# Kernel tuning notes

Hardware: AMD Instinct MI355X
Metric: run time of the kernel (lower is better)

## Reference

```python
import jax, jax.numpy as jnp
import numpy as np
import math

B, S, I, H = 64, 512, 512, 1024


def setup_inputs() -> dict:
    key = jax.random.key(0)
    kx, k1, k2, k3, k4 = jax.random.split(key, 5)
    stdv = 1.0 / math.sqrt(H)
    x = jax.random.normal(kx, (B, S, I), dtype=jnp.float32)
    w_ih = jax.random.uniform(k1, (4 * H, I), jnp.float32, -stdv, stdv)
    w_hh = jax.random.uniform(k2, (4 * H, H), jnp.float32, -stdv, stdv)
    b_ih = jax.random.uniform(k3, (4 * H,), jnp.float32, -stdv, stdv)
    b_hh = jax.random.uniform(k4, (4 * H,), jnp.float32, -stdv, stdv)
    return {"x": x, "w_ih": w_ih, "w_hh": w_hh, "b_ih": b_ih, "b_hh": b_hh}


def reference(x, w_ih, w_hh, b_ih, b_hh):
    # x: [B,S,I]; w_ih: [4H,I]; w_hh: [4H,H]; biases: [4H]
    Bsz, Ssz, _ = x.shape
    Hsz = w_hh.shape[1]
    # Precompute input contribution for all timesteps in one big GEMM.
    gx = jnp.einsum('bsi,gi->sbg', x, w_ih) + b_ih + b_hh  # [S,B,4H]

    def step(carry, gx_t):
        h, c = carry  # [B,H] each
        gates = gx_t + h @ w_hh.T  # [B,4H]
        i_t, f_t, g_t, o_t = jnp.split(gates, 4, axis=-1)
        i_t = jax.nn.sigmoid(i_t)
        f_t = jax.nn.sigmoid(f_t)
        g_t = jnp.tanh(g_t)
        o_t = jax.nn.sigmoid(o_t)
        c_new = f_t * c + i_t * g_t
        h_new = o_t * jnp.tanh(c_new)
        return (h_new, c_new), h_new

    h0 = jnp.zeros((Bsz, Hsz), dtype=x.dtype)
    c0 = jnp.zeros((Bsz, Hsz), dtype=x.dtype)
    (h_f, c_f), hidden_seq = jax.lax.scan(step, (h0, c0), gx)
    # hidden_seq: [S,B,H] (torch code cats along dim 0 of [1,B,H] slices)
    return hidden_seq, (h_f[None], c_f[None])
```

## Files before the change

### kernel.cpp

```cpp
#include <hip/hip_runtime.h>

typedef _Float16 f16;
typedef _Float16 f16x4 __attribute__((ext_vector_type(4)));
typedef _Float16 f16x8 __attribute__((ext_vector_type(8)));
typedef float f32x4 __attribute__((ext_vector_type(4)));

#define S_LEN 512
#define BSZ 64
#define ISZ 512
#define HSZ 1024

__device__ __forceinline__ float fast_sigmoid(float x) {
  return 1.f / (1.f + __expf(-x));
}
__device__ __forceinline__ float fast_tanh(float x) {
  float t = __expf(-2.f * fabsf(x));
  float r = (1.f - t) / (1.f + t);
  return copysignf(r, x);
}

template<int OFF>
__device__ __forceinline__ void ldg16_sc1(f16x8& d, const f16* p) {
  asm volatile("global_load_dwordx4 %0, %1, off offset:%2 sc1"
               : "=v"(d) : "v"(p), "i"(OFF));
}
__device__ __forceinline__ void st16_sc1(f16* p, f16x8 v) {
  asm volatile("global_store_dwordx4 %0, %1, off sc1" :: "v"(p), "v"(v) : "memory");
}
__device__ __forceinline__ int ld_flag_sc1(const int* p) {
  int v;
  asm volatile("global_load_dword %0, %1, off sc1\n\ts_waitcnt vmcnt(0)"
               : "=v"(v) : "v"(p) : "memory");
  return v;
}
__device__ __forceinline__ void st_flag_sc1(int* p, int v) {
  asm volatile("global_store_dword %0, %1, off sc1" :: "v"(p), "v"(v) : "memory");
}

__global__ void k_cvt(const float* __restrict__ src, f16* __restrict__ dst, int n4) {
  int i = blockIdx.x * blockDim.x + threadIdx.x;
  if (i < n4) {
    float4 v = ((const float4*)src)[i];
    f16x4 h = { (f16)v.x, (f16)v.y, (f16)v.z, (f16)v.w };
    ((f16x4*)dst)[i] = h;
  }
}

__global__ void k_pack_whh(const float* __restrict__ whh, f16* __restrict__ wp) {
  int i = blockIdx.x * blockDim.x + threadIdx.x;
  int idx4 = i * 4;
  int k = idx4 & (HSZ - 1);
  int P = idx4 >> 10;
  int cls = P & 3, u = (P >> 2) & 3, v = (P >> 4) & 7, w = P >> 7;
  int srow = cls * HSZ + w * 32 + v * 4 + u;
  float4 val = *(const float4*)&whh[(size_t)srow * HSZ + k];
  f16x4 h = { (f16)val.x, (f16)val.y, (f16)val.z, (f16)val.w };
  *(f16x4*)&wp[(size_t)P * HSZ + k] = h;
}

__global__ void k_misc(const float* __restrict__ bih, const float* __restrict__ bhh,
                       float* __restrict__ bsum, f16* __restrict__ hbuf,
                       int* __restrict__ bar) {
  int i = blockIdx.x * blockDim.x + threadIdx.x;
  if (i < 4096) bsum[i] = bih[i] + bhh[i];
  if (i < BSZ * HSZ) hbuf[i] = (f16)0.f;
  if (i < 1024) bar[i] = 0;
}

__global__ __launch_bounds__(256) void k_gemm_gx(
    const f16* __restrict__ xh, const f16* __restrict__ wh,
    const float* __restrict__ bsum, f16* __restrict__ gxp)
{
  __shared__ f16 As[128][40];
  __shared__ f16 Bs[128][40];
  const int bn = blockIdx.x, bm = blockIdx.y;
  const int tid = threadIdx.x;
  const int wid = tid >> 6, lane = tid & 63;
  const int wy = wid >> 1, wx = wid & 1;
  const int l15 = lane & 15, lq = lane >> 4;
  const int sr = tid >> 2, sc = (tid & 3) * 8;
  f32x4 acc[4][4] = {};
  const size_t arow = (size_t)bm * 128;
  const size_t brow = (size_t)bn * 128;
  for (int k0 = 0; k0 < ISZ; k0 += 32) {
    __syncthreads();
    *(f16x8*)&As[sr][sc]      = *(const f16x8*)&xh[(arow + sr) * ISZ + k0 + sc];
    *(f16x8*)&As[sr + 64][sc] = *(const f16x8*)&xh[(arow + sr + 64) * ISZ + k0 + sc];
    *(f16x8*)&Bs[sr][sc]      = *(const f16x8*)&wh[(brow + sr) * ISZ + k0 + sc];
    *(f16x8*)&Bs[sr + 64][sc] = *(const f16x8*)&wh[(brow + sr + 64) * ISZ + k0 + sc];
    __syncthreads();
    f16x8 af[4], bf[4];
    #pragma unroll
    for (int t = 0; t < 4; t++) af[t] = *(const f16x8*)&As[wy * 64 + t * 16 + l15][lq * 8];
    #pragma unroll
    for (int t = 0; t < 4; t++) bf[t] = *(const f16x8*)&Bs[wx * 64 + t * 16 + l15][lq * 8];
    #pragma unroll
    for (int mt = 0; mt < 4; mt++)
      #pragma unroll
      for (int nt = 0; nt < 4; nt++)
        acc[mt][nt] = __builtin_amdgcn_mfma_f32_16x16x32_f16(af[mt], bf[nt], acc[mt][nt], 0, 0, 0);
  }
  #pragma unroll
  for (int nt = 0; nt < 4; nt++) {
    const int n = bn * 128 + wx * 64 + nt * 16 + l15;
    const float bs = bsum[n];
    const int cls = n >> 10, j = n & 1023;
    const int w = j >> 5, v = (j >> 2) & 7, u = j & 3;
    #pragma unroll
    for (int mt = 0; mt < 4; mt++) {
      const int m0 = bm * 128 + wy * 64 + mt * 16 + lq * 4;
      #pragma unroll
      for (int r = 0; r < 4; r++) {
        const int m = m0 + r;
        const int b = m >> 9, s = m & 511;
        const int g = b >> 3, bl = b & 7;
        gxp[(((size_t)s * 8 + g) * 32 + w) * 1024 + v * 128 + bl * 16 + u * 4 + cls]
            = (f16)(acc[mt][nt][r] + bs);
      }
    }
  }
}

__global__ __launch_bounds__(512, 2) void k_lstm(
    const f16* __restrict__ wp, const f16* __restrict__ gxp,
    f16* __restrict__ hbuf, int* __restrict__ bar, float* __restrict__ out)
{
  __shared__ __align__(16) f16 hs[8192];
  __shared__ __align__(16) float pre[8][16][12];
  __shared__ __align__(16) f16 hpub[256];
  __shared__ f16 lds_pad[40960];
  const int wg = blockIdx.x;
  const int g  = wg & 7;
  const int w  = wg >> 3;
  const int tid = threadIdx.x;
  const int lane = tid & 63;
  const int wid = tid >> 6;
  const int l15 = lane & 15, lq = lane >> 4;
  const int hr = l15 & 7;
  int* flags = &bar[g * 32];
  lds_pad[tid] = (f16)0.f;

  f16x8 wv[32];
  {
    const f16* wsrc = wp + (size_t)(w * 128 + wid * 16 + l15) * HSZ + lq * 8;
    #pragma unroll
    for (int t = 0; t < 32; t++) wv[t] = *(const f16x8*)(wsrc + t * 32);
  }

  const int fidx = 2 * wid + (lane & 1) + ((lane >> 1) & 1) * 16;
  const int* fp = &flags[fidx];
  int* myflag = &flags[w];

  const int eb = lane >> 2, eu = lane & 3;
  float creg = 0.f;
  float hval = 0.f, cval = 0.f;
  const size_t hseq = (size_t)S_LEN * BSZ * HSZ;
  int p = 0;
  for (int s = 0; s < S_LEN; s++) {
    f16x4 gxv = {};
    if (lane < 32)
      gxv = *(const f16x4*)&gxp[(((size_t)s * 8 + g) * 32 + w) * 1024
                                + wid * 128 + lane * 4];
    for (;;) {
      int v = 0x7fffffff;
      if (lane < 4) v = ld_flag_sc1(fp);
      if (__all(v >= s)) break;
      __builtin_amdgcn_s_sleep(1);
    }
    {
      const f16* hsrc = hbuf + ((size_t)p * 8 + g) * 8192 + (size_t)tid * 8;
      f16x8 s0, s1;
      ldg16_sc1<0>(s0, hsrc);
      ldg16_sc1<0>(s1, hsrc + 4096);
      asm volatile("s_waitcnt vmcnt(0)" : "+v"(s0), "+v"(s1) :: "memory");
      *(f16x8*)&hs[tid * 8] = s0;
      *(f16x8*)&hs[tid * 8 + 4096] = s1;
    }
    asm volatile("s_waitcnt lgkmcnt(0)\n\ts_barrier" ::: "memory");
    f32x4 a0 = {}, a1 = {}, a2 = {}, a3 = {};
    #pragma unroll
    for (int t = 0; t < 32; t += 4) {
      f16x8 h0 = *(const f16x8*)&hs[(t + 0) * 256 + hr * 32 + lq * 8];
      f16x8 h1 = *(const f16x8*)&hs[(t + 1) * 256 + hr * 32 + lq * 8];
      f16x8 h2 = *(const f16x8*)&hs[(t + 2) * 256 + hr * 32 + lq * 8];
      f16x8 h3 = *(const f16x8*)&hs[(t + 3) * 256 + hr * 32 + lq * 8];
      a0 = __builtin_amdgcn_mfma_f32_16x16x32_f16(h0, wv[t + 0], a0, 0, 0, 0);
      a1 = __builtin_amdgcn_mfma_f32_16x16x32_f16(h1, wv[t + 1], a1, 0, 0, 0);
      a2 = __builtin_amdgcn_mfma_f32_16x16x32_f16(h2, wv[t + 2], a2, 0, 0, 0);
      a3 = __builtin_amdgcn_mfma_f32_16x16x32_f16(h3, wv[t + 3], a3, 0, 0, 0);
    }
    f32x4 accs = (a0 + a1) + (a2 + a3);
    if (lq < 2)
      *(f32x4*)&pre[wid][l15][lq * 4] = accs;
    asm volatile("s_waitcnt lgkmcnt(0)" ::: "memory");
    if (lane < 32) {
      const float p0 = pre[wid][eu * 4 + 0][eb] + (float)gxv[0];
      const float p1 = pre[wid][eu * 4 + 1][eb] + (float)gxv[1];
      const float p2 = pre[wid][eu * 4 + 2][eb] + (float)gxv[2];
      const float p3 = pre[wid][eu * 4 + 3][eb] + (float)gxv[3];
      const float ig = fast_sigmoid(p0);
      const float fg = fast_sigmoid(p1);
      const float gg = fast_tanh(p2);
      const float og = fast_sigmoid(p3);
      creg = fg * creg + ig * gg;
      const float h = og * fast_tanh(creg);
      hval = h; cval = creg;
      hpub[eb * 32 + wid * 4 + eu] = (f16)h;
      out[((size_t)s * BSZ + g * 8 + eb) * HSZ + w * 32 + wid * 4 + eu] = h;
      if (s == S_LEN - 1) {
        const int b = g * 8 + eb, J = w * 32 + wid * 4 + eu;
        out[hseq + (size_t)b * HSZ + J] = hval;
        out[hseq + (size_t)BSZ * HSZ + (size_t)b * HSZ + J] = cval;
      }
    }
    asm volatile("s_waitcnt lgkmcnt(0)\n\ts_barrier" ::: "memory");
    if (wid == 0 && s + 1 < S_LEN) {
      if (lane < 32) {
        f16x8 hv = *(const f16x8*)&hpub[lane * 8];
        st16_sc1(&hbuf[((size_t)(p ^ 1) * 8 + g) * 8192 + w * 256 + lane * 8], hv);
      }
      asm volatile("s_waitcnt vmcnt(0)" ::: "memory");
      if (lane == 0) st_flag_sc1(myflag, s + 1);
    }
    p ^= 1;
  }
}

extern "C" void kernel_launch(void* const* d_in, const int* in_sizes, int n_in,
                              void* d_out, int out_size, void* d_ws, size_t ws_size,
                              hipStream_t stream) {
  const float* x   = (const float*)d_in[0];
  const float* wih = (const float*)d_in[1];
  const float* whh = (const float*)d_in[2];
  const float* bih = (const float*)d_in[3];
  const float* bhh = (const float*)d_in[4];
  float* out = (float*)d_out;
  char* ws = (char*)d_ws;
  f16*   xh    = (f16*)(ws + 0);
  f16*   wih_h = (f16*)(ws + 33554432);
  f16*   wp    = (f16*)(ws + 37748736);
  float* bsum  = (float*)(ws + 46137344);
  f16*   hbuf  = (f16*)(ws + 46153728);
  f16*   gxp   = (f16*)(ws + 46415872);
  int*   bar   = (int*)(ws + 314851328);

  k_cvt<<<16384, 256, 0, stream>>>(x, xh, (BSZ * S_LEN * ISZ) / 4);
  k_cvt<<<2048, 256, 0, stream>>>(wih, wih_h, (4 * HSZ * ISZ) / 4);
  k_pack_whh<<<4096, 256, 0, stream>>>(whh, wp);
  k_misc<<<256, 256, 0, stream>>>(bih, bhh, bsum, hbuf, bar);
  dim3 g1(32, 256);
  k_gemm_gx<<<g1, 256, 0, stream>>>(xh, wih_h, bsum, gxp);
  void* args[] = { (void*)&wp, (void*)&gxp, (void*)&hbuf, (void*)&bar, (void*)&out };
  hipLaunchCooperativeKernel((void*)k_lstm, dim3(256), dim3(512), args, 0, stream);
}
```

Baseline: 2.592 ms.

## Split LSTM recurrent GEMM along K across waves, load h fragments directly from global

Each wave now owns a K-slice of the hidden state and computes all 128 gate columns for that slice. It loads its A-fragments directly from the global h buffer into registers instead of staging the whole h vector through LDS, and it issues the gx load alongside them. Partial sums from all 8 waves are reduced through a larger LDS buffer plus a cross-half shuffle. This removes the global-to-LDS copy, one barrier and the LDS padding used to cap occupancy, but adds a cross-wave reduction and reorganises the flag polling.

```diff
diff --git a/kernel.cpp b/kernel.cpp
--- a/kernel.cpp
+++ b/kernel.cpp
@@ -4,6 +4,7 @@
 typedef _Float16 f16x4 __attribute__((ext_vector_type(4)));
 typedef _Float16 f16x8 __attribute__((ext_vector_type(8)));
 typedef float f32x4 __attribute__((ext_vector_type(4)));
+typedef int i32x2 __attribute__((ext_vector_type(2)));
 
 #define S_LEN 512
 #define BSZ 64
@@ -19,11 +20,6 @@
   return copysignf(r, x);
 }
 
-template<int OFF>
-__device__ __forceinline__ void ldg16_sc1(f16x8& d, const f16* p) {
-  asm volatile("global_load_dwordx4 %0, %1, off offset:%2 sc1"
-               : "=v"(d) : "v"(p), "i"(OFF));
-}
 __device__ __forceinline__ void st16_sc1(f16* p, f16x8 v) {
   asm volatile("global_store_dwordx4 %0, %1, off sc1" :: "v"(p), "v"(v) : "memory");
 }
@@ -35,6 +31,18 @@
 }
 __device__ __forceinline__ void st_flag_sc1(int* p, int v) {
   asm volatile("global_store_dword %0, %1, off sc1" :: "v"(p), "v"(v) : "memory");
+}
+__device__ __forceinline__ void ld_afrags(f16x8& a0, f16x8& a1, f16x8& a2, f16x8& a3,
+                                          i32x2& gx, const f16* ap, const f16* gp) {
+  asm volatile(
+    "global_load_dwordx4 %0, %5, off sc1\n\t"
+    "global_load_dwordx4 %1, %5, off offset:512 sc1\n\t"
+    "global_load_dwordx4 %2, %5, off offset:1024 sc1\n\t"
+    "global_load_dwordx4 %3, %5, off offset:1536 sc1\n\t"
+    "global_load_dwordx2 %4, %6, off\n\t"
+    "s_waitcnt vmcnt(1)"
+    : "=&v"(a0), "=&v"(a1), "=&v"(a2), "=&v"(a3), "=&v"(gx)
+    : "v"(ap), "v"(gp) : "memory");
 }
 
 __global__ void k_cvt(const float* __restrict__ src, f16* __restrict__ dst, int n4) {
@@ -125,10 +133,8 @@
     const f16* __restrict__ wp, const f16* __restrict__ gxp,
     f16* __restrict__ hbuf, int* __restrict__ bar, float* __restrict__ out)
 {
-  __shared__ __align__(16) f16 hs[8192];
-  __shared__ __align__(16) float pre[8][16][12];
+  __shared__ __align__(16) float pre[8][128][12];
   __shared__ __align__(16) f16 hpub[256];
-  __shared__ f16 lds_pad[40960];
   const int wg = blockIdx.x;
   const int g  = wg & 7;
   const int w  = wg >> 3;
@@ -136,81 +142,87 @@
   const int lane = tid & 63;
   const int wid = tid >> 6;
   const int l15 = lane & 15, lq = lane >> 4;
-  const int hr = l15 & 7;
+  const int hr8 = l15 & 7;
   int* flags = &bar[g * 32];
-  lds_pad[tid] = (f16)0.f;
 
   f16x8 wv[32];
   {
-    const f16* wsrc = wp + (size_t)(w * 128 + wid * 16 + l15) * HSZ + lq * 8;
-    #pragma unroll
-    for (int t = 0; t < 32; t++) wv[t] = *(const f16x8*)(wsrc + t * 32);
-  }
-
-  const int fidx = 2 * wid + (lane & 1) + ((lane >> 1) & 1) * 16;
-  const int* fp = &flags[fidx];
+    const f16* wsrc = wp + (size_t)(w * 128 + l15) * HSZ + wid * 128 + lq * 8;
+    #pragma unroll
+    for (int nt = 0; nt < 8; nt++)
+      #pragma unroll
+      for (int kk = 0; kk < 4; kk++)
+        wv[nt * 4 + kk] = *(const f16x8*)(wsrc + (size_t)nt * 16 * HSZ + kk * 32);
+  }
+
+  const int* fp = &flags[wid * 4 + (lane & 3)];
   int* myflag = &flags[w];
 
-  const int eb = lane >> 2, eu = lane & 3;
+  const int vb = (lane >> 5) * 4;
+  const int ee = lane & 31;
+  const int eb = ee >> 2, eu = ee & 3;
+  const int n0 = wid * 16 + eu * 4;
   float creg = 0.f;
-  float hval = 0.f, cval = 0.f;
   const size_t hseq = (size_t)S_LEN * BSZ * HSZ;
   int p = 0;
   for (int s = 0; s < S_LEN; s++) {
-    f16x4 gxv = {};
-    if (lane < 32)
-      gxv = *(const f16x4*)&gxp[(((size_t)s * 8 + g) * 32 + w) * 1024
-                                + wid * 128 + lane * 4];
+    #pragma unroll
+    for (int t = 0; t < 32; t++) asm volatile("" : "+v"(wv[t]));
     for (;;) {
       int v = 0x7fffffff;
       if (lane < 4) v = ld_flag_sc1(fp);
       if (__all(v >= s)) break;
       __builtin_amdgcn_s_sleep(1);
     }
+    f16x8 a0, a1, a2, a3;
+    i32x2 gxr;
     {
-      const f16* hsrc = hbuf + ((size_t)p * 8 + g) * 8192 + (size_t)tid * 8;
-      f16x8 s0, s1;
-      ldg16_sc1<0>(s0, hsrc);
-      ldg16_sc1<0>(s1, hsrc + 4096);
-      asm volatile("s_waitcnt vmcnt(0)" : "+v"(s0), "+v"(s1) :: "memory");
-      *(f16x8*)&hs[tid * 8] = s0;
-      *(f16x8*)&hs[tid * 8 + 4096] = s1;
-    }
+      const f16* ap = hbuf + ((size_t)p * 8 + g) * 8192 + (size_t)(wid * 4) * 256
+                    + hr8 * 32 + lq * 8;
+      const f16* gp = &gxp[(((size_t)s * 8 + g) * 32 + w) * 1024 + wid * 128 + (lane & 31) * 4];
+      ld_afrags(a0, a1, a2, a3, gxr, ap, gp);
+    }
+    f32x4 acc[8] = {};
+    #pragma unroll
+    for (int nt = 0; nt < 8; nt++) acc[nt] = __builtin_amdgcn_mfma_f32_16x16x32_f16(a0, wv[nt * 4 + 0], acc[nt], 0, 0, 0);
+    #pragma unroll
+    for (int nt = 0; nt < 8; nt++) acc[nt] = __builtin_amdgcn_mfma_f32_16x16x32_f16(a1, wv[nt * 4 + 1], acc[nt], 0, 0, 0);
+    #pragma unroll
+    for (int nt = 0; nt < 8; nt++) acc[nt] = __builtin_amdgcn_mfma_f32_16x16x32_f16(a2, wv[nt * 4 + 2], acc[nt], 0, 0, 0);
+    #pragma unroll
+    for (int nt = 0; nt < 8; nt++) acc[nt] = __builtin_amdgcn_mfma_f32_16x16x32_f16(a3, wv[nt * 4 + 3], acc[nt], 0, 0, 0);
+    if (lq < 2)
+      #pragma unroll
+      for (int nt = 0; nt < 8; nt++)
+        *(f32x4*)&pre[wid][nt * 16 + l15][lq * 4] = acc[nt];
     asm volatile("s_waitcnt lgkmcnt(0)\n\ts_barrier" ::: "memory");
-    f32x4 a0 = {}, a1 = {}, a2 = {}, a3 = {};
-    #pragma unroll
-    for (int t = 0; t < 32; t += 4) {
-      f16x8 h0 = *(const f16x8*)&hs[(t + 0) * 256 + hr * 32 + lq * 8];
-      f16x8 h1 = *(const f16x8*)&hs[(t + 1) * 256 + hr * 32 + lq * 8];
-      f16x8 h2 = *(const f16x8*)&hs[(t + 2) * 256 + hr * 32 + lq * 8];
-      f16x8 h3 = *(const f16x8*)&hs[(t + 3) * 256 + hr * 32 + lq * 8];
-      a0 = __builtin_amdgcn_mfma_f32_16x16x32_f16(h0, wv[t + 0], a0, 0, 0, 0);
-      a1 = __builtin_amdgcn_mfma_f32_16x16x32_f16(h1, wv[t + 1], a1, 0, 0, 0);
-      a2 = __builtin_amdgcn_mfma_f32_16x16x32_f16(h2, wv[t + 2], a2, 0, 0, 0);
-      a3 = __builtin_amdgcn_mfma_f32_16x16x32_f16(h3, wv[t + 3], a3, 0, 0, 0);
-    }
-    f32x4 accs = (a0 + a1) + (a2 + a3);
-    if (lq < 2)
-      *(f32x4*)&pre[wid][l15][lq * 4] = accs;
-    asm volatile("s_waitcnt lgkmcnt(0)" ::: "memory");
+    asm volatile("s_waitcnt vmcnt(0)" : "+v"(gxr) :: "memory");
+    const f16x4 gxv = __builtin_bit_cast(f16x4, gxr);
+    float q0 = 0.f, q1 = 0.f, q2 = 0.f, q3 = 0.f;
+    #pragma unroll
+    for (int vi = 0; vi < 4; vi++) {
+      q0 += pre[vb + vi][n0 + 0][eb];
+      q1 += pre[vb + vi][n0 + 1][eb];
+      q2 += pre[vb + vi][n0 + 2][eb];
+      q3 += pre[vb + vi][n0 + 3][eb];
+    }
+    q0 += __shfl_xor(q0, 32);
+    q1 += __shfl_xor(q1, 32);
+    q2 += __shfl_xor(q2, 32);
+    q3 += __shfl_xor(q3, 32);
     if (lane < 32) {
-      const float p0 = pre[wid][eu * 4 + 0][eb] + (float)gxv[0];
-      const float p1 = pre[wid][eu * 4 + 1][eb] + (float)gxv[1];
-      const float p2 = pre[wid][eu * 4 + 2][eb] + (float)gxv[2];
-      const float p3 = pre[wid][eu * 4 + 3][eb] + (float)gxv[3];
-      const float ig = fast_sigmoid(p0);
-      const float fg = fast_sigmoid(p1);
-      const float gg = fast_tanh(p2);
-      const float og = fast_sigmoid(p3);
+      const float ig = fast_sigmoid(q0 + (float)gxv[0]);
+      const float fg = fast_sigmoid(q1 + (float)gxv[1]);
+      const float gg = fast_tanh(q2 + (float)gxv[2]);
+      const float og = fast_sigmoid(q3 + (float)gxv[3]);
       creg = fg * creg + ig * gg;
       const float h = og * fast_tanh(creg);
-      hval = h; cval = creg;
       hpub[eb * 32 + wid * 4 + eu] = (f16)h;
       out[((size_t)s * BSZ + g * 8 + eb) * HSZ + w * 32 + wid * 4 + eu] = h;
       if (s == S_LEN - 1) {
         const int b = g * 8 + eb, J = w * 32 + wid * 4 + eu;
-        out[hseq + (size_t)b * HSZ + J] = hval;
-        out[hseq + (size_t)BSZ * HSZ + (size_t)b * HSZ + J] = cval;
+        out[hseq + (size_t)b * HSZ + J] = h;
+        out[hseq + (size_t)BSZ * HSZ + (size_t)b * HSZ + J] = creg;
       }
     }
     asm volatile("s_waitcnt lgkmcnt(0)\n\ts_barrier" ::: "memory");
```

New measurement: 5.069 ms. 1.96x slower.

## Replace flag barrier with sentinel-tagged hidden-state data polling over 4-slot ring

Applied to the files above, without the earlier changes.

Drops the separate per-group flag array. Consumers now poll the hidden-state buffer itself until no 0xFFFF sentinel words remain, using a 4-deep ring of h slots. Each consumer re-poisons the slot it used one step earlier. This removes the store-wait-flag-store round trip and the extra flag load latency on the serial recurrence critical path. It also removes the LDS padding array, which allows higher occupancy. The cost is polling 32 bytes per thread, and correctness relies on the fp16 h value never encoding as 0xFFFF (a NaN bit pattern).

```diff
diff --git a/kernel.cpp b/kernel.cpp
--- a/kernel.cpp
+++ b/kernel.cpp
@@ -4,6 +4,8 @@
 typedef _Float16 f16x4 __attribute__((ext_vector_type(4)));
 typedef _Float16 f16x8 __attribute__((ext_vector_type(8)));
 typedef float f32x4 __attribute__((ext_vector_type(4)));
+typedef int i32x4 __attribute__((ext_vector_type(4)));
+typedef unsigned short ushort4v __attribute__((ext_vector_type(4)));
 
 #define S_LEN 512
 #define BSZ 64
@@ -19,22 +21,16 @@
   return copysignf(r, x);
 }
 
-template<int OFF>
-__device__ __forceinline__ void ldg16_sc1(f16x8& d, const f16* p) {
-  asm volatile("global_load_dwordx4 %0, %1, off offset:%2 sc1"
-               : "=v"(d) : "v"(p), "i"(OFF));
-}
 __device__ __forceinline__ void st16_sc1(f16* p, f16x8 v) {
   asm volatile("global_store_dwordx4 %0, %1, off sc1" :: "v"(p), "v"(v) : "memory");
 }
-__device__ __forceinline__ int ld_flag_sc1(const int* p) {
-  int v;
-  asm volatile("global_load_dword %0, %1, off sc1\n\ts_waitcnt vmcnt(0)"
-               : "=v"(v) : "v"(p) : "memory");
-  return v;
-}
-__device__ __forceinline__ void st_flag_sc1(int* p, int v) {
-  asm volatile("global_store_dword %0, %1, off sc1" :: "v"(p), "v"(v) : "memory");
+__device__ __forceinline__ void ld2x16_sc1(f16x8& d0, f16x8& d1,
+                                           const f16* p0, const f16* p1) {
+  asm volatile(
+    "global_load_dwordx4 %0, %2, off sc1\n\t"
+    "global_load_dwordx4 %1, %3, off sc1\n\t"
+    "s_waitcnt vmcnt(0)"
+    : "=&v"(d0), "=&v"(d1) : "v"(p0), "v"(p1) : "memory");
 }
 
 __global__ void k_cvt(const float* __restrict__ src, f16* __restrict__ dst, int n4) {
@@ -59,12 +55,12 @@
 }
 
 __global__ void k_misc(const float* __restrict__ bih, const float* __restrict__ bhh,
-                       float* __restrict__ bsum, f16* __restrict__ hbuf,
-                       int* __restrict__ bar) {
+                       float* __restrict__ bsum, f16* __restrict__ hbuf) {
   int i = blockIdx.x * blockDim.x + threadIdx.x;
   if (i < 4096) bsum[i] = bih[i] + bhh[i];
-  if (i < BSZ * HSZ) hbuf[i] = (f16)0.f;
-  if (i < 1024) bar[i] = 0;
+  unsigned short v = (i >= 16384) ? 0xFFFFu : 0u;
+  ushort4v q = { v, v, v, v };
+  ((ushort4v*)hbuf)[i] = q;
 }
 
 __global__ __launch_bounds__(256) void k_gemm_gx(
@@ -123,12 +119,11 @@
 
 __global__ __launch_bounds__(512, 2) void k_lstm(
     const f16* __restrict__ wp, const f16* __restrict__ gxp,
-    f16* __restrict__ hbuf, int* __restrict__ bar, float* __restrict__ out)
+    f16* __restrict__ hbuf, float* __restrict__ out)
 {
   __shared__ __align__(16) f16 hs[8192];
   __shared__ __align__(16) float pre[8][16][12];
   __shared__ __align__(16) f16 hpub[256];
-  __shared__ f16 lds_pad[40960];
   const int wg = blockIdx.x;
   const int g  = wg & 7;
   const int w  = wg >> 3;
@@ -137,8 +132,6 @@
   const int wid = tid >> 6;
   const int l15 = lane & 15, lq = lane >> 4;
   const int hr = l15 & 7;
-  int* flags = &bar[g * 32];
-  lds_pad[tid] = (f16)0.f;
 
   f16x8 wv[32];
   {
@@ -147,36 +140,34 @@
     for (int t = 0; t < 32; t++) wv[t] = *(const f16x8*)(wsrc + t * 32);
   }
 
-  const int fidx = 2 * wid + (lane & 1) + ((lane >> 1) & 1) * 16;
-  const int* fp = &flags[fidx];
-  int* myflag = &flags[w];
-
+  const f16x8 sentinel16 = __builtin_bit_cast(f16x8, (i32x4){-1, -1, -1, -1});
   const int eb = lane >> 2, eu = lane & 3;
   float creg = 0.f;
-  float hval = 0.f, cval = 0.f;
   const size_t hseq = (size_t)S_LEN * BSZ * HSZ;
-  int p = 0;
   for (int s = 0; s < S_LEN; s++) {
     f16x4 gxv = {};
     if (lane < 32)
       gxv = *(const f16x4*)&gxp[(((size_t)s * 8 + g) * 32 + w) * 1024
                                 + wid * 128 + lane * 4];
-    for (;;) {
-      int v = 0x7fffffff;
-      if (lane < 4) v = ld_flag_sc1(fp);
-      if (__all(v >= s)) break;
-      __builtin_amdgcn_s_sleep(1);
-    }
+    f16x8 s0v, s1v;
     {
-      const f16* hsrc = hbuf + ((size_t)p * 8 + g) * 8192 + (size_t)tid * 8;
-      f16x8 s0, s1;
-      ldg16_sc1<0>(s0, hsrc);
-      ldg16_sc1<0>(s1, hsrc + 4096);
-      asm volatile("s_waitcnt vmcnt(0)" : "+v"(s0), "+v"(s1) :: "memory");
-      *(f16x8*)&hs[tid * 8] = s0;
-      *(f16x8*)&hs[tid * 8 + 4096] = s1;
+      const f16* hsrc = hbuf + ((size_t)(s & 3) * 8 + g) * 8192 + (size_t)tid * 8;
+      for (;;) {
+        ld2x16_sc1(s0v, s1v, hsrc, hsrc + 4096);
+        i32x4 u0 = __builtin_bit_cast(i32x4, s0v);
+        i32x4 u1 = __builtin_bit_cast(i32x4, s1v);
+        bool ok = (u0[0] != -1) && (u0[1] != -1) && (u0[2] != -1) && (u0[3] != -1)
+               && (u1[0] != -1) && (u1[1] != -1) && (u1[2] != -1) && (u1[3] != -1);
+        if (__all(ok)) break;
+        __builtin_amdgcn_s_sleep(1);
+      }
+      *(f16x8*)&hs[tid * 8] = s0v;
+      *(f16x8*)&hs[tid * 8 + 4096] = s1v;
     }
     asm volatile("s_waitcnt lgkmcnt(0)\n\ts_barrier" ::: "memory");
+    if (s > 0 && wid == 7 && lane < 32)
+      st16_sc1(&hbuf[((size_t)((s - 1) & 3) * 8 + g) * 8192 + w * 256 + lane * 8],
+               sentinel16);
     f32x4 a0 = {}, a1 = {}, a2 = {}, a3 = {};
     #pragma unroll
     for (int t = 0; t < 32; t += 4) {
@@ -193,6 +184,7 @@
     if (lq < 2)
       *(f32x4*)&pre[wid][l15][lq * 4] = accs;
     asm volatile("s_waitcnt lgkmcnt(0)" ::: "memory");
+    if (wid == 7) asm volatile("s_waitcnt vmcnt(0)" ::: "memory");
     if (lane < 32) {
       const float p0 = pre[wid][eu * 4 + 0][eb] + (float)gxv[0];
       const float p1 = pre[wid][eu * 4 + 1][eb] + (float)gxv[1];
@@ -204,25 +196,19 @@
       const float og = fast_sigmoid(p3);
       creg = fg * creg + ig * gg;
       const float h = og * fast_tanh(creg);
-      hval = h; cval = creg;
       hpub[eb * 32 + wid * 4 + eu] = (f16)h;
       out[((size_t)s * BSZ + g * 8 + eb) * HSZ + w * 32 + wid * 4 + eu] = h;
       if (s == S_LEN - 1) {
         const int b = g * 8 + eb, J = w * 32 + wid * 4 + eu;
-        out[hseq + (size_t)b * HSZ + J] = hval;
-        out[hseq + (size_t)BSZ * HSZ + (size_t)b * HSZ + J] = cval;
+        out[hseq + (size_t)b * HSZ + J] = h;
+        out[hseq + (size_t)BSZ * HSZ + (size_t)b * HSZ + J] = creg;
       }
     }
     asm volatile("s_waitcnt lgkmcnt(0)\n\ts_barrier" ::: "memory");
-    if (wid == 0 && s + 1 < S_LEN) {
-      if (lane < 32) {
-        f16x8 hv = *(const f16x8*)&hpub[lane * 8];
-        st16_sc1(&hbuf[((size_t)(p ^ 1) * 8 + g) * 8192 + w * 256 + lane * 8], hv);
-      }
-      asm volatile("s_waitcnt vmcnt(0)" ::: "memory");
-      if (lane == 0) st_flag_sc1(myflag, s + 1);
-    }
-    p ^= 1;
+    if (wid == 0 && s + 1 < S_LEN && lane < 32) {
+      f16x8 hv = *(const f16x8*)&hpub[lane * 8];
+      st16_sc1(&hbuf[((size_t)((s + 1) & 3) * 8 + g) * 8192 + w * 256 + lane * 8], hv);
+    }
   }
 }
 
@@ -241,15 +227,14 @@
   f16*   wp    = (f16*)(ws + 37748736);
   float* bsum  = (float*)(ws + 46137344);
   f16*   hbuf  = (f16*)(ws + 46153728);
-  f16*   gxp   = (f16*)(ws + 46415872);
-  int*   bar   = (int*)(ws + 314851328);
+  f16*   gxp   = (f16*)(ws + 46678016);
 
   k_cvt<<<16384, 256, 0, stream>>>(x, xh, (BSZ * S_LEN * ISZ) / 4);
   k_cvt<<<2048, 256, 0, stream>>>(wih, wih_h, (4 * HSZ * ISZ) / 4);
   k_pack_whh<<<4096, 256, 0, stream>>>(whh, wp);
-  k_misc<<<256, 256, 0, stream>>>(bih, bhh, bsum, hbuf, bar);
+  k_misc<<<256, 256, 0, stream>>>(bih, bhh, bsum, hbuf);
   dim3 g1(32, 256);
   k_gemm_gx<<<g1, 256, 0, stream>>>(xh, wih_h, bsum, gxp);
-  void* args[] = { (void*)&wp, (void*)&gxp, (void*)&hbuf, (void*)&bar, (void*)&out };
+  void* args[] = { (void*)&wp, (void*)&gxp, (void*)&hbuf, (void*)&out };
   hipLaunchCooperativeKernel((void*)k_lstm, dim3(256), dim3(512), args, 0, stream);
 }
```

Result: faster. 2.319 ms (-10.5%).
